# Kernel tuning notes

Hardware: AMD Instinct MI355X
Metric: run time of the kernel (lower is better)

Reference implementation:

```python
import jax, jax.numpy as jnp
import numpy as np

L, B, N, D = 8, 2, 512, 1024      # ensemble size, batch, seq, model dim
H, DH = 8, 64                      # heads, dim_head
INNER = H * DH
M = 2 * L                          # messages = [tokens, ensemble_out] concatenated on dim 0
SCALE = DH ** -0.5


def rmsnorm(x, w, eps):
    return x * jax.lax.rsqrt(jnp.mean(x * x, axis=-1, keepdims=True) + eps) * w


def setup_inputs() -> dict:
    key = jax.random.key(0)
    ks = jax.random.split(key, 8)
    bound = D ** -0.5
    tokens = jax.random.normal(ks[0], (L, B, N, D), dtype=jnp.float32)
    # per-member Linear(dim, dim): torch weight [out,in] -> stored [L, D, D]
    w_net = jax.random.uniform(ks[1], (L, D, D), jnp.float32, -bound, bound)
    b_net = jnp.zeros((L, D), jnp.float32)
    # voting attention params (stored transposed so x @ W works)
    norm_w = jnp.ones((D,), jnp.float32)
    knorm_w = jnp.ones((DH,), jnp.float32)
    wq = jax.random.uniform(ks[2], (D, INNER), jnp.float32, -bound, bound)
    wkv = jax.random.uniform(ks[3], (D, 2 * INNER), jnp.float32, -bound, bound)
    wg = jax.random.uniform(ks[4], (D, H), jnp.float32, -bound, bound)
    wout = jax.random.uniform(ks[5], (INNER, D), jnp.float32, -(INNER ** -0.5), INNER ** -0.5)
    return dict(tokens=tokens, w_net=w_net, b_net=b_net, norm_w=norm_w,
                wq=wq, wkv=wkv, knorm_w=knorm_w, wg=wg, wout=wout)


def reference(tokens, w_net, b_net, norm_w, wq, wkv, knorm_w, wg, wout):
    eps = jnp.finfo(tokens.dtype).eps
    # vmapped sub-network: per-member Linear
    out = jnp.einsum('lbnd,lod->lbno', tokens, w_net) + b_net[:, None, None, :]
    # messages = cat([tokens, out], dim=0) -> context of M=2L messages per (b,n)
    ctx = jnp.concatenate([tokens, out], axis=0)            # [M,B,N,D]
    # voting attention: queries are the tokens (len-1 per position), kv over M messages.
    # original tiles ctx over l ('m b ... d -> (lq b) ... m d'); we broadcast instead.
    tn = rmsnorm(tokens, norm_w, eps)                        # query norm only
    q = (tn @ wq).reshape(L, B, N, H, DH)
    kv = ctx @ wkv                                           # [M,B,N,2*INNER]
    k, v = jnp.split(kv, 2, axis=-1)
    k = rmsnorm(k.reshape(M, B, N, H, DH), knorm_w, eps)
    v = v.reshape(M, B, N, H, DH)
    sim = jnp.einsum('lbnhd,mbnhd->lbnhm', q, k) * SCALE
    attn = jax.nn.softmax(sim, axis=-1)
    o = jnp.einsum('lbnhm,mbnhd->lbnhd', attn, v)
    gates = jax.nn.sigmoid(tn @ wg)                          # [L,B,N,H]
    o = o * gates[..., None]
    pooled = o.reshape(L, B, N, INNER) @ wout                # [L,B,N,D]
    return pooled
```

## Files before the change

### kernel.cpp

```cpp
#include <hip/hip_runtime.h>
#include <hip/hip_bf16.h>
#include <math.h>

#define L_ 8
#define B_ 2
#define N_ 512
#define D_ 1024
#define H_ 8
#define DH_ 64
#define INNER_ 512
#define M_ 16
#define BN_TOK 1024
#define EPS 1.1920928955078125e-07f
#define SCALE_ 0.125f

typedef __attribute__((ext_vector_type(8))) __bf16 bf16x8;
typedef __attribute__((ext_vector_type(4))) __bf16 bf16x4;
typedef __attribute__((ext_vector_type(4))) float f32x4;

#define BARF() do { __builtin_amdgcn_s_barrier(); __builtin_amdgcn_sched_barrier(0); } while (0)
#define LGKM0() do { asm volatile("s_waitcnt lgkmcnt(0)" ::: "memory"); \
                     __builtin_amdgcn_sched_barrier(0); } while (0)
#define GLL(SRC, DST) __builtin_amdgcn_global_load_lds( \
    (const __attribute__((address_space(1))) void*)(SRC), \
    (__attribute__((address_space(3))) void*)(DST), 16, 0, 0)

__device__ void transpose_body(const float* __restrict__ in,
                               __bf16* __restrict__ out, int R, int C,
                               int bx, int by)
{
    __shared__ float tile[32][33];
    const int x = threadIdx.x & 31, y = threadIdx.x >> 5;
    #pragma unroll
    for (int r = 0; r < 4; ++r)
        tile[y + r * 8][x] = in[(size_t)(by * 32 + y + r * 8) * C + bx * 32 + x];
    __syncthreads();
    #pragma unroll
    for (int r = 0; r < 4; ++r)
        out[(size_t)(bx * 32 + y + r * 8) * R + by * 32 + x] = (__bf16)tile[x][y + r * 8];
}

__global__ __launch_bounds__(256) void prep_kernel(
    const float* __restrict__ tokens, const float* __restrict__ norm_w,
    const float* __restrict__ w_net, const float* __restrict__ wq,
    const float* __restrict__ wkv, const float* __restrict__ wout,
    const float* __restrict__ wg,
    __bf16* __restrict__ tok_bf, __bf16* __restrict__ tn_bf,
    __bf16* __restrict__ wnet_bf, __bf16* __restrict__ wqt,
    __bf16* __restrict__ wkvt, __bf16* __restrict__ woutt,
    __bf16* __restrict__ wgT)
{
    const int bid = blockIdx.x;
    const int t = threadIdx.x;

    if (bid < 8192) {
        const int wave = t >> 6, lane = t & 63;
        __shared__ float wsum[4];
        const float4 v = ((const float4*)(tokens + (size_t)bid * D_))[t];
        float ss = fmaf(v.x, v.x, fmaf(v.y, v.y, fmaf(v.z, v.z, v.w * v.w)));
        #pragma unroll
        for (int o = 1; o < 64; o <<= 1) ss += __shfl_xor(ss, o);
        if (lane == 0) wsum[wave] = ss;
        __syncthreads();
        const float rsv = rsqrtf((wsum[0] + wsum[1] + wsum[2] + wsum[3]) * (1.f / D_) + EPS);
        const float4 nw = ((const float4*)norm_w)[t];
        bf16x4 tb; tb.x = (__bf16)v.x; tb.y = (__bf16)v.y; tb.z = (__bf16)v.z; tb.w = (__bf16)v.w;
        ((bf16x4*)(tok_bf + (size_t)bid * D_))[t] = tb;
        bf16x4 nb;
        nb.x = (__bf16)(v.x * rsv * nw.x); nb.y = (__bf16)(v.y * rsv * nw.y);
        nb.z = (__bf16)(v.z * rsv * nw.z); nb.w = (__bf16)(v.w * rsv * nw.w);
        ((bf16x4*)(tn_bf + (size_t)bid * D_))[t] = nb;
    } else if (bid < 10240) {
        const int base = (bid - 8192) * 1024 + t;
        #pragma unroll
        for (int j = 0; j < 4; ++j) {
            const int i = base + j * 256;
            float4 v = ((const float4*)w_net)[i];
            bf16x4 o;
            o.x = (__bf16)v.x; o.y = (__bf16)v.y; o.z = (__bf16)v.z; o.w = (__bf16)v.w;
            *(bf16x4*)(wnet_bf + (size_t)i * 4) = o;
        }
    } else if (bid < 12288) {
        const int b2 = bid - 10240;
        if (b2 < 512)        transpose_body(wq, wqt, 1024, 512, b2 & 15, b2 >> 4);
        else if (b2 < 1536)  { const int b3 = b2 - 512;  transpose_body(wkv, wkvt, 1024, 1024, b3 & 31, b3 >> 5); }
        else                 { const int b3 = b2 - 1536; transpose_body(wout, woutt, 512, 1024, b3 & 31, b3 >> 5); }
    } else {
        const int g = (bid - 12288) * 256 + t;
        const int h = g >> 10, d = g & 1023;
        wgT[g] = (h < 8) ? (__bf16)wg[d * 8 + h] : (__bf16)0.f;
    }
}

__global__ __launch_bounds__(512, 2) void gemm_fused(
    const __bf16* __restrict__ tok, const __bf16* __restrict__ tn,
    const __bf16* __restrict__ wnet, const __bf16* __restrict__ wqt,
    const float* __restrict__ bias, const __bf16* __restrict__ wgT,
    __bf16* __restrict__ out_bf, __bf16* __restrict__ q_bf,
    float* __restrict__ gates_out)
{
    __shared__ __align__(16) __bf16 As[2][256 * 64];
    __shared__ __align__(16) __bf16 Bs[2][256 * 64];

    constexpr int NT = 16, K = 1024;
    const int tid = threadIdx.x;
    const int w = tid >> 6, lane = tid & 63;
    const int fr = lane & 15, fq = lane >> 4;
    const int bid = blockIdx.x;

    if (bid >= 192) {
        const int r0 = ((bid - 192) * 8 + w) * 16;
        const __bf16* arow = tn + (size_t)(r0 + fr) * D_ + fq * 8;
        const __bf16* brow = wgT + (size_t)fr * D_ + fq * 8;
        f32x4 gacc = (f32x4){0.f, 0.f, 0.f, 0.f};
        #pragma unroll 8
        for (int k0 = 0; k0 < D_; k0 += 32) {
            bf16x8 a = *(const bf16x8*)(arow + k0);
            bf16x8 b = *(const bf16x8*)(brow + k0);
            gacc = __builtin_amdgcn_mfma_f32_16x16x32_bf16(a, b, gacc, 0, 0, 0);
        }
        if (fr < 8) {
            #pragma unroll
            for (int r = 0; r < 4; ++r)
                gates_out[(size_t)(r0 + fq * 4 + r) * H_ + fr] = 1.f / (1.f + expf(-gacc[r]));
        }
        return;
    }

    const int wm = w >> 2, wn = w & 3;
    const bool isq = bid >= 128;
    const int b2 = isq ? bid - 128 : bid;
    const int ntx = isq ? 2 : 4;
    const int c = b2 & 7, s = b2 >> 3;
    const int sq = s / ntx;
    const int m0 = (c * 4 + sq) * 256;
    const int n0 = (s - sq * ntx) * 256;
    const __bf16* Ab;
    const __bf16* Btb;
    const float* biasp = nullptr;
    int Ncols;
    if (isq) {
        Ab = tn + (size_t)m0 * K; Btb = wqt + (size_t)n0 * K; Ncols = 512;
    } else {
        Ab = tok + (size_t)m0 * K;
        Btb = wnet + (size_t)(m0 >> 10) * 1024 * K + (size_t)n0 * K;
        Ncols = 1024;
        biasp = bias + (size_t)(m0 >> 10) * 1024;
    }

    const int lrow = lane >> 3;
    const int lchunk = (lane & 7) ^ lrow;
    const int fo0 = ((fq ^ (lane & 7)) << 4);
    const int fo1 = (((4 + fq) ^ (lane & 7)) << 4);

#define STAGE_A(T2, PB, HALF) do {                                            \
    _Pragma("unroll")                                                         \
    for (int ld = (HALF) * 2; ld < (HALF) * 2 + 2; ++ld)                      \
        GLL(Ab + (size_t)(w * 32 + ld * 8 + lrow) * K + (T2) * 64 + lchunk * 8, \
            &As[PB][(w * 32 + ld * 8) * 64]);                                 \
} while (0)
#define STAGE_B(T2, PB, HALF) do {                                            \
    _Pragma("unroll")                                                         \
    for (int ld = (HALF) * 2; ld < (HALF) * 2 + 2; ++ld)                      \
        GLL(Btb + (size_t)(w * 32 + ld * 8 + lrow) * K + (T2) * 64 + lchunk * 8, \
            &Bs[PB][(w * 32 + ld * 8) * 64]);                                 \
} while (0)
#define RD_A(DST, MIOFF, FO) do {                                             \
    _Pragma("unroll")                                                         \
    for (int mi = 0; mi < 4; ++mi)                                            \
        (DST)[mi] = *(const bf16x8*)(Ap + ((wm * 128 + ((MIOFF) + mi) * 16 + fr) << 7) + (FO)); \
} while (0)
#define RD_B(DST, FO) do {                                                    \
    _Pragma("unroll")                                                         \
    for (int nj = 0; nj < 4; ++nj)                                            \
        (DST)[nj] = *(const bf16x8*)(Bp + ((wn * 64 + nj * 16 + fr) << 7) + (FO)); \
} while (0)
#define MFMA16(AFR, BFR, AOFF) do {                                           \
    _Pragma("unroll")                                                         \
    for (int mi = 0; mi < 4; ++mi)                                            \
        _Pragma("unroll")                                                     \
        for (int nj = 0; nj < 4; ++nj)                                        \
            acc[(AOFF) + mi][nj] = __builtin_amdgcn_mfma_f32_16x16x32_bf16(   \
                (AFR)[mi], (BFR)[nj], acc[(AOFF) + mi][nj], 0, 0, 0);         \
} while (0)

    f32x4 acc[8][4];
    #pragma unroll
    for (int mi = 0; mi < 8; ++mi)
        #pragma unroll
        for (int nj = 0; nj < 4; ++nj)
            acc[mi][nj] = (f32x4){0.f, 0.f, 0.f, 0.f};

    STAGE_A(0, 0, 0); STAGE_A(0, 0, 1);
    STAGE_B(0, 0, 0); STAGE_B(0, 0, 1);
    STAGE_A(1, 1, 0); STAGE_A(1, 1, 1);
    asm volatile("s_waitcnt vmcnt(4)" ::: "memory");
    BARF();

    for (int t = 0; t < NT; ++t) {
        const int p = t & 1;
        const char* Ap = (const char*)&As[p][0];
        const char* Bp = (const char*)&Bs[p][0];
        bf16x8 am0k0[4], am1k0[4], bk0[4], am0k1[4], am1k1[4], bk1[4];

        RD_A(am0k0, 0, fo0); RD_B(bk0, fo0); RD_A(am1k0, 4, fo0);
        if (t + 1 < NT) STAGE_B(t + 1, p ^ 1, 0);
        BARF();
        __builtin_amdgcn_s_setprio(1);
        MFMA16(am0k0, bk0, 0);
        __builtin_amdgcn_s_setprio(0);
        BARF();

        RD_A(am0k1, 0, fo1); RD_B(bk1, fo1); RD_A(am1k1, 4, fo1);
        if (t + 1 < NT) STAGE_B(t + 1, p ^ 1, 1);
        BARF();
        __builtin_amdgcn_s_setprio(1);
        MFMA16(am1k0, bk0, 4);
        __builtin_amdgcn_s_setprio(0);
        LGKM0();
        BARF();

        if (t + 2 < NT) STAGE_A(t + 2, p, 0);
        __builtin_amdgcn_s_setprio(1);
        MFMA16(am0k1, bk1, 0);
        __builtin_amdgcn_s_setprio(0);
        BARF();

        if (t + 2 < NT) STAGE_A(t + 2, p, 1);
        __builtin_amdgcn_s_setprio(1);
        MFMA16(am1k1, bk1, 4);
        __builtin_amdgcn_s_setprio(0);
        if (t + 2 < NT) { asm volatile("s_waitcnt vmcnt(4)" ::: "memory"); }
        else            { asm volatile("s_waitcnt vmcnt(0)" ::: "memory"); }
        BARF();
    }

    #pragma unroll
    for (int mi = 0; mi < 8; ++mi) {
        const int r0 = m0 + wm * 128 + mi * 16 + fq * 4;
        #pragma unroll
        for (int nj = 0; nj < 4; ++nj) {
            const int col = n0 + wn * 64 + nj * 16 + fr;
            const float badd = (biasp != nullptr) ? biasp[col] : 0.f;
            __bf16* Co = isq ? q_bf : out_bf;
            #pragma unroll
            for (int r = 0; r < 4; ++r)
                Co[(size_t)(r0 + r) * Ncols + col] = (__bf16)(acc[mi][nj][r] + badd);
        }
    }
#undef STAGE_A
#undef STAGE_B
#undef RD_A
#undef RD_B
#undef MFMA16
}

__global__ __launch_bounds__(512, 2) void gemm_kv(
    const __bf16* __restrict__ tok, const __bf16* __restrict__ outm,
    const __bf16* __restrict__ wkvt, __bf16* __restrict__ kv_bf)
{
    __shared__ __align__(16) __bf16 As[2][256 * 64];
    __shared__ __align__(16) __bf16 Bs[2][256 * 64];
    constexpr int NT = 16, K = 1024, Ncols = 1024;
    const int tid = threadIdx.x;
    const int w = tid >> 6, lane = tid & 63;
    const int wm = w >> 2, wn = w & 3;
    const int fr = lane & 15, fq = lane >> 4;
    const int bid = blockIdx.x;
    const int c = bid & 7, s = bid >> 3;
    const int sq = s >> 2;
    const int m0 = (c * 8 + sq) * 256;
    const int n0 = (s - sq * 4) * 256;
    const __bf16* Ab = (m0 >= 8192) ? (outm + (size_t)(m0 - 8192) * K)
                                    : (tok + (size_t)m0 * K);
    const __bf16* Btb = wkvt + (size_t)n0 * K;

    const int lrow = lane >> 3;
    const int lchunk = (lane & 7) ^ lrow;
    const int fo0 = ((fq ^ (lane & 7)) << 4);
    const int fo1 = (((4 + fq) ^ (lane & 7)) << 4);

#define STAGE_A(T2, PB, HALF) do {                                            \
    _Pragma("unroll")                                                         \
    for (int ld = (HALF) * 2; ld < (HALF) * 2 + 2; ++ld)                      \
        GLL(Ab + (size_t)(w * 32 + ld * 8 + lrow) * K + (T2) * 64 + lchunk * 8, \
            &As[PB][(w * 32 + ld * 8) * 64]);                                 \
} while (0)
#define STAGE_B(T2, PB, HALF) do {                                            \
    _Pragma("unroll")                                                         \
    for (int ld = (HALF) * 2; ld < (HALF) * 2 + 2; ++ld)                      \
        GLL(Btb + (size_t)(w * 32 + ld * 8 + lrow) * K + (T2) * 64 + lchunk * 8, \
            &Bs[PB][(w * 32 + ld * 8) * 64]);                                 \
} while (0)
#define RD_A(DST, MIOFF, FO) do {                                             \
    _Pragma("unroll")                                                         \
    for (int mi = 0; mi < 4; ++mi)                                            \
        (DST)[mi] = *(const bf16x8*)(Ap + ((wm * 128 + ((MIOFF) + mi) * 16 + fr) << 7) + (FO)); \
} while (0)
#define RD_B(DST, FO) do {                                                    \
    _Pragma("unroll")                                                         \
    for (int nj = 0; nj < 4; ++nj)                                            \
        (DST)[nj] = *(const bf16x8*)(Bp + ((wn * 64 + nj * 16 + fr) << 7) + (FO)); \
} while (0)
#define MFMA16(AFR, BFR, AOFF) do {                                           \
    _Pragma("unroll")                                                         \
    for (int mi = 0; mi < 4; ++mi)                                            \
        _Pragma("unroll")                                                     \
        for (int nj = 0; nj < 4; ++nj)                                        \
            acc[(AOFF) + mi][nj] = __builtin_amdgcn_mfma_f32_16x16x32_bf16(   \
                (AFR)[mi], (BFR)[nj], acc[(AOFF) + mi][nj], 0, 0, 0);         \
} while (0)

    f32x4 acc[8][4];
    #pragma unroll
    for (int mi = 0; mi < 8; ++mi)
        #pragma unroll
        for (int nj = 0; nj < 4; ++nj)
            acc[mi][nj] = (f32x4){0.f, 0.f, 0.f, 0.f};

    STAGE_A(0, 0, 0); STAGE_A(0, 0, 1);
    STAGE_B(0, 0, 0); STAGE_B(0, 0, 1);
    STAGE_A(1, 1, 0); STAGE_A(1, 1, 1);
    asm volatile("s_waitcnt vmcnt(4)" ::: "memory");
    BARF();

    for (int t = 0; t < NT; ++t) {
        const int p = t & 1;
        const char* Ap = (const char*)&As[p][0];
        const char* Bp = (const char*)&Bs[p][0];
        bf16x8 am0k0[4], am1k0[4], bk0[4], am0k1[4], am1k1[4], bk1[4];

        RD_A(am0k0, 0, fo0); RD_B(bk0, fo0); RD_A(am1k0, 4, fo0);
        if (t + 1 < NT) STAGE_B(t + 1, p ^ 1, 0);
        BARF();
        __builtin_amdgcn_s_setprio(1);
        MFMA16(am0k0, bk0, 0);
        __builtin_amdgcn_s_setprio(0);
        BARF();

        RD_A(am0k1, 0, fo1); RD_B(bk1, fo1); RD_A(am1k1, 4, fo1);
        if (t + 1 < NT) STAGE_B(t + 1, p ^ 1, 1);
        BARF();
        __builtin_amdgcn_s_setprio(1);
        MFMA16(am1k0, bk0, 4);
        __builtin_amdgcn_s_setprio(0);
        LGKM0();
        BARF();

        if (t + 2 < NT) STAGE_A(t + 2, p, 0);
        __builtin_amdgcn_s_setprio(1);
        MFMA16(am0k1, bk1, 0);
        __builtin_amdgcn_s_setprio(0);
        BARF();

        if (t + 2 < NT) STAGE_A(t + 2, p, 1);
        __builtin_amdgcn_s_setprio(1);
        MFMA16(am1k1, bk1, 4);
        __builtin_amdgcn_s_setprio(0);
        if (t + 2 < NT) { asm volatile("s_waitcnt vmcnt(4)" ::: "memory"); }
        else            { asm volatile("s_waitcnt vmcnt(0)" ::: "memory"); }
        BARF();
    }

    #pragma unroll
    for (int mi = 0; mi < 8; ++mi) {
        const int r0 = m0 + wm * 128 + mi * 16 + fq * 4;
        #pragma unroll
        for (int nj = 0; nj < 4; ++nj) {
            const int col = n0 + wn * 64 + nj * 16 + fr;
            #pragma unroll
            for (int r = 0; r < 4; ++r)
                kv_bf[(size_t)(r0 + r) * Ncols + col] = (__bf16)acc[mi][nj][r];
        }
    }
#undef STAGE_A
#undef STAGE_B
#undef RD_A
#undef RD_B
#undef MFMA16
}

__global__ __launch_bounds__(512, 2) void gemm_final(
    const __bf16* __restrict__ A,
    const __bf16* __restrict__ Bt,
    float* __restrict__ Cf)
{
    __shared__ __align__(16) __bf16 As[2][256 * 64];
    __shared__ __align__(16) __bf16 Bs[2][128 * 64];
    constexpr int NT = 8, K = 512, Ncols = 1024;
    const int tid = threadIdx.x;
    const int w = tid >> 6, lane = tid & 63;
    const int wm = w >> 1, wn = w & 1;
    const int fr = lane & 15, fq = lane >> 4;
    const int bid = blockIdx.x;
    const int c = bid & 7, s = bid >> 3;
    const int sq = s >> 3;
    const int m0 = (c * 4 + sq) * 256;
    const int n0 = (s - sq * 8) * 128;
    const __bf16* Ab = A + (size_t)m0 * K;
    const __bf16* Btb = Bt + (size_t)n0 * K;

    const int lrow = lane >> 3;
    const int lchunk = (lane & 7) ^ lrow;
    const int fo0 = ((fq ^ (lane & 7)) << 4);
    const int fo1 = (((4 + fq) ^ (lane & 7)) << 4);

#define STAGE_A(T2, PB, HALF) do {                                            \
    _Pragma("unroll")                                                         \
    for (int ld = (HALF) * 2; ld < (HALF) * 2 + 2; ++ld)                      \
        GLL(Ab + (size_t)(w * 32 + ld * 8 + lrow) * K + (T2) * 64 + lchunk * 8, \
            &As[PB][(w * 32 + ld * 8) * 64]);                                 \
} while (0)
#define STAGE_B(T2, PB, HALF)                                                 \
    GLL(Btb + (size_t)(w * 16 + (HALF) * 8 + lrow) * K + (T2) * 64 + lchunk * 8, \
        &Bs[PB][(w * 16 + (HALF) * 8) * 64])
#define RD_A(DST, FO) do {                                                    \
    _Pragma("unroll")                                                         \
    for (int mi = 0; mi < 4; ++mi)                                            \
        (DST)[mi] = *(const bf16x8*)(Ap + ((wm * 64 + mi * 16 + fr) << 7) + (FO)); \
} while (0)
#define RD_B(DST, FO) do {                                                    \
    _Pragma("unroll")                                                         \
    for (int nj = 0; nj < 4; ++nj)                                            \
        (DST)[nj] = *(const bf16x8*)(Bp + ((wn * 64 + nj * 16 + fr) << 7) + (FO)); \
} while (0)
#define MFMA16C1(AFR, BFR) do {                                               \
    _Pragma("unroll")                                                         \
    for (int mi = 0; mi < 4; ++mi)                                            \
        _Pragma("unroll")                                                     \
        for (int nj = 0; nj < 4; ++nj)                                        \
            acc[mi][nj] = __builtin_amdgcn_mfma_f32_16x16x32_bf16(            \
                (AFR)[mi], (BFR)[nj], acc[mi][nj], 0, 0, 0);                  \
} while (0)

    f32x4 acc[4][4];
    #pragma unroll
    for (int mi = 0; mi < 4; ++mi)
        #pragma unroll
        for (int nj = 0; nj < 4; ++nj)
            acc[mi][nj] = (f32x4){0.f, 0.f, 0.f, 0.f};

    STAGE_A(0, 0, 0); STAGE_A(0, 0, 1);
    STAGE_B(0, 0, 0); STAGE_B(0, 0, 1);
    STAGE_A(1, 1, 0); STAGE_A(1, 1, 1);
    asm volatile("s_waitcnt vmcnt(4)" ::: "memory");
    BARF();

    for (int t = 0; t < NT; ++t) {
        const int p = t & 1;
        const char* Ap = (const char*)&As[p][0];
        const char* Bp = (const char*)&Bs[p][0];
        bf16x8 ak0[4], bk0[4], ak1[4], bk1[4];

        RD_A(ak0, fo0); RD_B(bk0, fo0);
        if (t + 1 < NT) STAGE_B(t + 1, p ^ 1, 0);
        BARF();
        __builtin_amdgcn_s_setprio(1);
        MFMA16C1(ak0, bk0);
        __builtin_amdgcn_s_setprio(0);
        BARF();

        RD_A(ak1, fo1); RD_B(bk1, fo1);
        if (t + 1 < NT) STAGE_B(t + 1, p ^ 1, 1);
        BARF();
        __builtin_amdgcn_s_setprio(1);
        MFMA16C1(ak1, bk1);
        __builtin_amdgcn_s_setprio(0);
        LGKM0();
        BARF();

        if (t + 2 < NT) { STAGE_A(t + 2, p, 0); STAGE_A(t + 2, p, 1); }
        if (t + 2 < NT) { asm volatile("s_waitcnt vmcnt(4)" ::: "memory"); }
        else            { asm volatile("s_waitcnt vmcnt(0)" ::: "memory"); }
        BARF();
    }

    #pragma unroll
    for (int mi = 0; mi < 4; ++mi) {
        const int r0 = m0 + wm * 64 + mi * 16 + fq * 4;
        #pragma unroll
        for (int nj = 0; nj < 4; ++nj) {
            const int col = n0 + wn * 64 + nj * 16 + fr;
            #pragma unroll
            for (int r = 0; r < 4; ++r)
                Cf[(size_t)(r0 + r) * Ncols + col] = acc[mi][nj][r];
        }
    }
#undef STAGE_A
#undef STAGE_B
#undef RD_A
#undef RD_B
#undef MFMA16C1
}

__global__ __launch_bounds__(512) void attn_kernel(
    const __bf16* __restrict__ q,
    const __bf16* __restrict__ kv,
    const float* __restrict__ gates,
    const float* __restrict__ knw,
    __bf16* __restrict__ og)
{
    const int bn = blockIdx.x;
    const int tid = threadIdx.x;
    const int h = tid >> 6, lane = tid & 63;

    __shared__ __align__(16) __bf16 qs[8][520];
    __shared__ __align__(16) __bf16 kvs[16][1032];
    __shared__ float ssm[8][8][17];
    __shared__ float kn[64];
    __shared__ float gs[64];

    {
        const int l = tid >> 6, c8 = tid & 63;
        *(bf16x8*)&qs[l][c8 * 8] =
            *(const bf16x8*)(q + ((size_t)(l * BN_TOK + bn)) * INNER_ + c8 * 8);
    }
    #pragma unroll
    for (int i = 0; i < 4; ++i) {
        const int g = tid + i * 512;
        const int m = g >> 7, c8 = g & 127;
        *(bf16x8*)&kvs[m][c8 * 8] =
            *(const bf16x8*)(kv + ((size_t)(m * BN_TOK + bn)) * 1024 + c8 * 8);
    }
    if (tid < 64) {
        kn[tid] = knw[tid];
        gs[tid] = gates[((size_t)((tid >> 3) * BN_TOK + bn)) * H_ + (tid & 7)];
    }
    __syncthreads();

    const int m = lane & 15, grp = lane >> 4;

    float s2 = 0.f;
    #pragma unroll
    for (int j = 0; j < 16; ++j) {
        float v = (float)kvs[m][h * DH_ + grp * 16 + j];
        s2 = fmaf(v, v, s2);
    }
    s2 += __shfl_xor(s2, 16);
    s2 += __shfl_xor(s2, 32);
    const float kscale = rsqrtf(s2 * (1.f / DH_) + EPS) * SCALE_;

    const int l0 = grp, l1 = grp + 4;
    float sim0 = 0.f, sim1 = 0.f;
    #pragma unroll
    for (int d = 0; d < DH_; ++d) {
        const float kf = (float)kvs[m][h * DH_ + d] * kn[d];
        sim0 = fmaf((float)qs[l0][h * DH_ + d], kf, sim0);
        sim1 = fmaf((float)qs[l1][h * DH_ + d], kf, sim1);
    }
    sim0 *= kscale; sim1 *= kscale;

    float mx0 = sim0, mx1 = sim1;
    #pragma unroll
    for (int o = 1; o < 16; o <<= 1) {
        mx0 = fmaxf(mx0, __shfl_xor(mx0, o));
        mx1 = fmaxf(mx1, __shfl_xor(mx1, o));
    }
    float e0 = expf(sim0 - mx0), e1 = expf(sim1 - mx1);
    float sm0 = e0, sm1 = e1;
    #pragma unroll
    for (int o = 1; o < 16; o <<= 1) {
        sm0 += __shfl_xor(sm0, o);
        sm1 += __shfl_xor(sm1, o);
    }
    ssm[h][l0][m] = e0 / sm0;
    ssm[h][l1][m] = e1 / sm1;

    float vf[16];
    #pragma unroll
    for (int mm = 0; mm < 16; ++mm)
        vf[mm] = (float)kvs[mm][INNER_ + h * DH_ + lane];
    #pragma unroll
    for (int l = 0; l < 8; ++l) {
        float o = 0.f;
        #pragma unroll
        for (int mm = 0; mm < 16; ++mm) o = fmaf(ssm[h][l][mm], vf[mm], o);
        og[((size_t)(l * BN_TOK + bn)) * INNER_ + h * DH_ + lane] =
            (__bf16)(o * gs[l * 8 + h]);
    }
}

extern "C" void kernel_launch(void* const* d_in, const int* in_sizes, int n_in,
                              void* d_out, int out_size, void* d_ws, size_t ws_size,
                              hipStream_t stream)
{
    const float* tokens = (const float*)d_in[0];
    const float* w_net  = (const float*)d_in[1];
    const float* b_net  = (const float*)d_in[2];
    const float* norm_w = (const float*)d_in[3];
    const float* wq     = (const float*)d_in[4];
    const float* wkv    = (const float*)d_in[5];
    const float* knw    = (const float*)d_in[6];
    const float* wg     = (const float*)d_in[7];
    const float* wout   = (const float*)d_in[8];
    float* out = (float*)d_out;

    char* ws = (char*)d_ws;
    __bf16* tok_bf  = (__bf16*)(ws);
    __bf16* tn_bf   = (__bf16*)(ws + 16777216);
    __bf16* out_bf  = (__bf16*)(ws + 33554432);
    __bf16* q_bf    = (__bf16*)(ws + 50331648);
    __bf16* kv_bf   = (__bf16*)(ws + 58720256);
    __bf16* og_bf   = (__bf16*)(ws + 92274688);
    __bf16* wnet_bf = (__bf16*)(ws + 100663296);
    __bf16* wqt_bf  = (__bf16*)(ws + 117440512);
    __bf16* wkvt_bf = (__bf16*)(ws + 118489088);
    __bf16* woutt_bf= (__bf16*)(ws + 120586240);
    float*  ws_g    = (float*)(ws + 121667584);
    __bf16* wgT_bf  = (__bf16*)(ws + 121929728);

    prep_kernel<<<12352, 256, 0, stream>>>(tokens, norm_w, w_net, wq, wkv, wout, wg,
                                           tok_bf, tn_bf, wnet_bf, wqt_bf,
                                           wkvt_bf, woutt_bf, wgT_bf);
    gemm_fused<<<256, 512, 0, stream>>>(tok_bf, tn_bf, wnet_bf, wqt_bf, b_net,
                                        wgT_bf, out_bf, q_bf, ws_g);
    gemm_kv<<<256, 512, 0, stream>>>(tok_bf, out_bf, wkvt_bf, kv_bf);
    attn_kernel<<<BN_TOK, 512, 0, stream>>>(q_bf, kv_bf, ws_g, knw, og_bf);
    gemm_final<<<256, 512, 0, stream>>>(og_bf, woutt_bf, out);
}
```

Before: 126.2 us.

## Split GEMM LDS tiles into K-halves with finer-grained staging pipeline

The shared main-loop macros for gemm_fused and gemm_kv now store each 64-wide K tile as two 32-wide halves with a new XOR swizzle. The loop is restructured into four phases, each reading one A half-fragment and issuing one staged half-tile load, instead of preloading both K halves of fragments. This cuts register pressure for fragment buffers and interleaves the global-to-LDS loads more evenly with the MFMAs. In exchange it adds more barriers and lgkm waits per iteration, and B fragments are reloaded twice per half. gemm_final is only renamed.

After: 144.3 us. 14.4% more time.

```diff
diff --git a/kernel.cpp b/kernel.cpp
--- a/kernel.cpp
+++ b/kernel.cpp
@@ -92,6 +92,94 @@
     }
 }
 
+
+#define CFG0_DECL()                                                           \
+    __shared__ __align__(16) __bf16 As[2][2][256 * 32];           \
+    __shared__ __align__(16) __bf16 Bs[2][2][256 * 32];
+
+#define CFG0_LANES()                                                          \
+    const int schunk = (lane & 3) ^ ((lane >> 3) & 3);                        \
+    const int srow = (lane >> 2);                                             \
+    const int fsw = (fq ^ ((fr >> 1) & 3)) << 4;
+
+#define STAGE_A(T2, KH, PB) do {                                              \
+    _Pragma("unroll")                                                         \
+    for (int rd = 0; rd < 2; ++rd)                                            \
+        GLL(Ab + (size_t)(rd * 128 + w * 16 + srow) * K + (T2) * 64 + (KH) * 32 + schunk * 8, \
+            &As[PB][KH][(rd * 128 + w * 16) * 32]);                           \
+} while (0)
+#define STAGE_B(T2, KH, PB) do {                                              \
+    _Pragma("unroll")                                                         \
+    for (int rd = 0; rd < 2; ++rd)                                            \
+        GLL(Btb + (size_t)(rd * 128 + w * 16 + srow) * K + (T2) * 64 + (KH) * 32 + schunk * 8, \
+            &Bs[PB][KH][(rd * 128 + w * 16) * 32]);                           \
+} while (0)
+#define RD_A4(DST, MIOFF, KHP) do {                                           \
+    _Pragma("unroll")                                                         \
+    for (int mi = 0; mi < 4; ++mi)                                            \
+        (DST)[mi] = *(const bf16x8*)((KHP) + (((wm * 128 + ((MIOFF) + mi) * 16 + fr) << 6) + fsw)); \
+} while (0)
+#define RD_B4(DST, KHP) do {                                                  \
+    _Pragma("unroll")                                                         \
+    for (int nj = 0; nj < 4; ++nj)                                            \
+        (DST)[nj] = *(const bf16x8*)((KHP) + (((wn * 64 + nj * 16 + fr) << 6) + fsw)); \
+} while (0)
+#define MFMA16(AFR, BFR, AOFF) do {                                           \
+    _Pragma("unroll")                                                         \
+    for (int mi = 0; mi < 4; ++mi)                                            \
+        _Pragma("unroll")                                                     \
+        for (int nj = 0; nj < 4; ++nj)                                        \
+            acc[(AOFF) + mi][nj] = __builtin_amdgcn_mfma_f32_16x16x32_bf16(   \
+                (AFR)[mi], (BFR)[nj], acc[(AOFF) + mi][nj], 0, 0, 0);         \
+} while (0)
+
+#define CFG0_PROLOGUE()                                                       \
+    STAGE_A(0, 0, 0); STAGE_B(0, 0, 0);                                       \
+    STAGE_A(0, 1, 0); STAGE_B(0, 1, 0);                                       \
+    STAGE_A(1, 0, 1); STAGE_B(1, 0, 1);                                       \
+    asm volatile("s_waitcnt vmcnt(4)" ::: "memory");                          \
+    BARF();
+
+#define CFG0_LOOP(NTv)                                                        \
+    for (int t = 0; t < (NTv); ++t) {                                         \
+        const int p = t & 1;                                                  \
+        const char* A0p = (const char*)&As[p][0][0];                          \
+        const char* A1p = (const char*)&As[p][1][0];                          \
+        const char* B0p = (const char*)&Bs[p][0][0];                          \
+        const char* B1p = (const char*)&Bs[p][1][0];                          \
+        bf16x8 al[4], ah[4], bb[4];                                           \
+                         \
+        RD_A4(al, 0, A0p); RD_B4(bb, B0p);                                    \
+        if (t + 1 < (NTv)) STAGE_A(t + 1, 1, p ^ 1);                          \
+        BARF(); LGKM0();                                                      \
+        __builtin_amdgcn_s_setprio(1); MFMA16(al, bb, 0);                     \
+        __builtin_amdgcn_s_setprio(0);                                        \
+        BARF();                                                               \
+                                \
+        RD_A4(ah, 4, A0p);                                                    \
+        if (t + 1 < (NTv)) STAGE_B(t + 1, 1, p ^ 1);                          \
+        BARF(); LGKM0();                                                      \
+        __builtin_amdgcn_s_setprio(1); MFMA16(ah, bb, 4);                     \
+        __builtin_amdgcn_s_setprio(0);                                        \
+        BARF();                                                               \
+          \
+        RD_A4(al, 0, A1p); RD_B4(bb, B1p);                                    \
+        if (t + 2 < (NTv)) STAGE_A(t + 2, 0, p);                              \
+        BARF(); LGKM0();                                                      \
+        __builtin_amdgcn_s_setprio(1); MFMA16(al, bb, 0);                     \
+        __builtin_amdgcn_s_setprio(0);                                        \
+        BARF();                                                               \
+                \
+        RD_A4(ah, 4, A1p);                                                    \
+        if (t + 2 < (NTv)) STAGE_B(t + 2, 0, p);                              \
+        BARF(); LGKM0();                                                      \
+        __builtin_amdgcn_s_setprio(1); MFMA16(ah, bb, 4);                     \
+        __builtin_amdgcn_s_setprio(0);                                        \
+        if (t + 2 < (NTv))      { asm volatile("s_waitcnt vmcnt(4)" ::: "memory"); } \
+        else if (t + 1 < (NTv)) { asm volatile("s_waitcnt vmcnt(0)" ::: "memory"); } \
+        BARF();                                                               \
+    }
+
 __global__ __launch_bounds__(512, 2) void gemm_fused(
     const __bf16* __restrict__ tok, const __bf16* __restrict__ tn,
     const __bf16* __restrict__ wnet, const __bf16* __restrict__ wqt,
@@ -99,9 +187,7 @@
     __bf16* __restrict__ out_bf, __bf16* __restrict__ q_bf,
     float* __restrict__ gates_out)
 {
-    __shared__ __align__(16) __bf16 As[2][256 * 64];
-    __shared__ __align__(16) __bf16 Bs[2][256 * 64];
-
+    CFG0_DECL();
     constexpr int NT = 16, K = 1024;
     const int tid = threadIdx.x;
     const int w = tid >> 6, lane = tid & 63;
@@ -148,42 +234,7 @@
         biasp = bias + (size_t)(m0 >> 10) * 1024;
     }
 
-    const int lrow = lane >> 3;
-    const int lchunk = (lane & 7) ^ lrow;
-    const int fo0 = ((fq ^ (lane & 7)) << 4);
-    const int fo1 = (((4 + fq) ^ (lane & 7)) << 4);
-
-#define STAGE_A(T2, PB, HALF) do {                                            \
-    _Pragma("unroll")                                                         \
-    for (int ld = (HALF) * 2; ld < (HALF) * 2 + 2; ++ld)                      \
-        GLL(Ab + (size_t)(w * 32 + ld * 8 + lrow) * K + (T2) * 64 + lchunk * 8, \
-            &As[PB][(w * 32 + ld * 8) * 64]);                                 \
-} while (0)
-#define STAGE_B(T2, PB, HALF) do {                                            \
-    _Pragma("unroll")                                                         \
-    for (int ld = (HALF) * 2; ld < (HALF) * 2 + 2; ++ld)                      \
-        GLL(Btb + (size_t)(w * 32 + ld * 8 + lrow) * K + (T2) * 64 + lchunk * 8, \
-            &Bs[PB][(w * 32 + ld * 8) * 64]);                                 \
-} while (0)
-#define RD_A(DST, MIOFF, FO) do {                                             \
-    _Pragma("unroll")                                                         \
-    for (int mi = 0; mi < 4; ++mi)                                            \
-        (DST)[mi] = *(const bf16x8*)(Ap + ((wm * 128 + ((MIOFF) + mi) * 16 + fr) << 7) + (FO)); \
-} while (0)
-#define RD_B(DST, FO) do {                                                    \
-    _Pragma("unroll")                                                         \
-    for (int nj = 0; nj < 4; ++nj)                                            \
-        (DST)[nj] = *(const bf16x8*)(Bp + ((wn * 64 + nj * 16 + fr) << 7) + (FO)); \
-} while (0)
-#define MFMA16(AFR, BFR, AOFF) do {                                           \
-    _Pragma("unroll")                                                         \
-    for (int mi = 0; mi < 4; ++mi)                                            \
-        _Pragma("unroll")                                                     \
-        for (int nj = 0; nj < 4; ++nj)                                        \
-            acc[(AOFF) + mi][nj] = __builtin_amdgcn_mfma_f32_16x16x32_bf16(   \
-                (AFR)[mi], (BFR)[nj], acc[(AOFF) + mi][nj], 0, 0, 0);         \
-} while (0)
-
+    CFG0_LANES();
     f32x4 acc[8][4];
     #pragma unroll
     for (int mi = 0; mi < 8; ++mi)
@@ -191,49 +242,8 @@
         for (int nj = 0; nj < 4; ++nj)
             acc[mi][nj] = (f32x4){0.f, 0.f, 0.f, 0.f};
 
-    STAGE_A(0, 0, 0); STAGE_A(0, 0, 1);
-    STAGE_B(0, 0, 0); STAGE_B(0, 0, 1);
-    STAGE_A(1, 1, 0); STAGE_A(1, 1, 1);
-    asm volatile("s_waitcnt vmcnt(4)" ::: "memory");
-    BARF();
-
-    for (int t = 0; t < NT; ++t) {
-        const int p = t & 1;
-        const char* Ap = (const char*)&As[p][0];
-        const char* Bp = (const char*)&Bs[p][0];
-        bf16x8 am0k0[4], am1k0[4], bk0[4], am0k1[4], am1k1[4], bk1[4];
-
-        RD_A(am0k0, 0, fo0); RD_B(bk0, fo0); RD_A(am1k0, 4, fo0);
-        if (t + 1 < NT) STAGE_B(t + 1, p ^ 1, 0);
-        BARF();
-        __builtin_amdgcn_s_setprio(1);
-        MFMA16(am0k0, bk0, 0);
-        __builtin_amdgcn_s_setprio(0);
-        BARF();
-
-        RD_A(am0k1, 0, fo1); RD_B(bk1, fo1); RD_A(am1k1, 4, fo1);
-        if (t + 1 < NT) STAGE_B(t + 1, p ^ 1, 1);
-        BARF();
-        __builtin_amdgcn_s_setprio(1);
-        MFMA16(am1k0, bk0, 4);
-        __builtin_amdgcn_s_setprio(0);
-        LGKM0();
-        BARF();
-
-        if (t + 2 < NT) STAGE_A(t + 2, p, 0);
-        __builtin_amdgcn_s_setprio(1);
-        MFMA16(am0k1, bk1, 0);
-        __builtin_amdgcn_s_setprio(0);
-        BARF();
-
-        if (t + 2 < NT) STAGE_A(t + 2, p, 1);
-        __builtin_amdgcn_s_setprio(1);
-        MFMA16(am1k1, bk1, 4);
-        __builtin_amdgcn_s_setprio(0);
-        if (t + 2 < NT) { asm volatile("s_waitcnt vmcnt(4)" ::: "memory"); }
-        else            { asm volatile("s_waitcnt vmcnt(0)" ::: "memory"); }
-        BARF();
-    }
+    CFG0_PROLOGUE();
+    CFG0_LOOP(NT);
 
     #pragma unroll
     for (int mi = 0; mi < 8; ++mi) {
@@ -248,19 +258,13 @@
                 Co[(size_t)(r0 + r) * Ncols + col] = (__bf16)(acc[mi][nj][r] + badd);
         }
     }
-#undef STAGE_A
-#undef STAGE_B
-#undef RD_A
-#undef RD_B
-#undef MFMA16
 }
 
 __global__ __launch_bounds__(512, 2) void gemm_kv(
     const __bf16* __restrict__ tok, const __bf16* __restrict__ outm,
     const __bf16* __restrict__ wkvt, __bf16* __restrict__ kv_bf)
 {
-    __shared__ __align__(16) __bf16 As[2][256 * 64];
-    __shared__ __align__(16) __bf16 Bs[2][256 * 64];
+    CFG0_DECL();
     constexpr int NT = 16, K = 1024, Ncols = 1024;
     const int tid = threadIdx.x;
     const int w = tid >> 6, lane = tid & 63;
@@ -275,42 +279,7 @@
                                     : (tok + (size_t)m0 * K);
     const __bf16* Btb = wkvt + (size_t)n0 * K;
 
-    const int lrow = lane >> 3;
-    const int lchunk = (lane & 7) ^ lrow;
-    const int fo0 = ((fq ^ (lane & 7)) << 4);
-    const int fo1 = (((4 + fq) ^ (lane & 7)) << 4);
-
-#define STAGE_A(T2, PB, HALF) do {                                            \
-    _Pragma("unroll")                                                         \
-    for (int ld = (HALF) * 2; ld < (HALF) * 2 + 2; ++ld)                      \
-        GLL(Ab + (size_t)(w * 32 + ld * 8 + lrow) * K + (T2) * 64 + lchunk * 8, \
-            &As[PB][(w * 32 + ld * 8) * 64]);                                 \
-} while (0)
-#define STAGE_B(T2, PB, HALF) do {                                            \
-    _Pragma("unroll")                                                         \
-    for (int ld = (HALF) * 2; ld < (HALF) * 2 + 2; ++ld)                      \
-        GLL(Btb + (size_t)(w * 32 + ld * 8 + lrow) * K + (T2) * 64 + lchunk * 8, \
-            &Bs[PB][(w * 32 + ld * 8) * 64]);                                 \
-} while (0)
-#define RD_A(DST, MIOFF, FO) do {                                             \
-    _Pragma("unroll")                                                         \
-    for (int mi = 0; mi < 4; ++mi)                                            \
-        (DST)[mi] = *(const bf16x8*)(Ap + ((wm * 128 + ((MIOFF) + mi) * 16 + fr) << 7) + (FO)); \
-} while (0)
-#define RD_B(DST, FO) do {                                                    \
-    _Pragma("unroll")                                                         \
-    for (int nj = 0; nj < 4; ++nj)                                            \
-        (DST)[nj] = *(const bf16x8*)(Bp + ((wn * 64 + nj * 16 + fr) << 7) + (FO)); \
-} while (0)
-#define MFMA16(AFR, BFR, AOFF) do {                                           \
-    _Pragma("unroll")                                                         \
-    for (int mi = 0; mi < 4; ++mi)                                            \
-        _Pragma("unroll")                                                     \
-        for (int nj = 0; nj < 4; ++nj)                                        \
-            acc[(AOFF) + mi][nj] = __builtin_amdgcn_mfma_f32_16x16x32_bf16(   \
-                (AFR)[mi], (BFR)[nj], acc[(AOFF) + mi][nj], 0, 0, 0);         \
-} while (0)
-
+    CFG0_LANES();
     f32x4 acc[8][4];
     #pragma unroll
     for (int mi = 0; mi < 8; ++mi)
@@ -318,49 +287,8 @@
         for (int nj = 0; nj < 4; ++nj)
             acc[mi][nj] = (f32x4){0.f, 0.f, 0.f, 0.f};
 
-    STAGE_A(0, 0, 0); STAGE_A(0, 0, 1);
-    STAGE_B(0, 0, 0); STAGE_B(0, 0, 1);
-    STAGE_A(1, 1, 0); STAGE_A(1, 1, 1);
-    asm volatile("s_waitcnt vmcnt(4)" ::: "memory");
-    BARF();
-
-    for (int t = 0; t < NT; ++t) {
-        const int p = t & 1;
-        const char* Ap = (const char*)&As[p][0];
-        const char* Bp = (const char*)&Bs[p][0];
-        bf16x8 am0k0[4], am1k0[4], bk0[4], am0k1[4], am1k1[4], bk1[4];
-
-        RD_A(am0k0, 0, fo0); RD_B(bk0, fo0); RD_A(am1k0, 4, fo0);
-        if (t + 1 < NT) STAGE_B(t + 1, p ^ 1, 0);
-        BARF();
-        __builtin_amdgcn_s_setprio(1);
-        MFMA16(am0k0, bk0, 0);
-        __builtin_amdgcn_s_setprio(0);
-        BARF();
-
-        RD_A(am0k1, 0, fo1); RD_B(bk1, fo1); RD_A(am1k1, 4, fo1);
-        if (t + 1 < NT) STAGE_B(t + 1, p ^ 1, 1);
-        BARF();
-        __builtin_amdgcn_s_setprio(1);
-        MFMA16(am1k0, bk0, 4);
-        __builtin_amdgcn_s_setprio(0);
-        LGKM0();
-        BARF();
-
-        if (t + 2 < NT) STAGE_A(t + 2, p, 0);
-        __builtin_amdgcn_s_setprio(1);
-        MFMA16(am0k1, bk1, 0);
-        __builtin_amdgcn_s_setprio(0);
-        BARF();
-
-        if (t + 2 < NT) STAGE_A(t + 2, p, 1);
-        __builtin_amdgcn_s_setprio(1);
-        MFMA16(am1k1, bk1, 4);
-        __builtin_amdgcn_s_setprio(0);
-        if (t + 2 < NT) { asm volatile("s_waitcnt vmcnt(4)" ::: "memory"); }
-        else            { asm volatile("s_waitcnt vmcnt(0)" ::: "memory"); }
-        BARF();
-    }
+    CFG0_PROLOGUE();
+    CFG0_LOOP(NT);
 
     #pragma unroll
     for (int mi = 0; mi < 8; ++mi) {
@@ -373,20 +301,18 @@
                 kv_bf[(size_t)(r0 + r) * Ncols + col] = (__bf16)acc[mi][nj][r];
         }
     }
+}
+
 #undef STAGE_A
 #undef STAGE_B
-#undef RD_A
-#undef RD_B
-#undef MFMA16
-}
 
 __global__ __launch_bounds__(512, 2) void gemm_final(
     const __bf16* __restrict__ A,
     const __bf16* __restrict__ Bt,
     float* __restrict__ Cf)
 {
-    __shared__ __align__(16) __bf16 As[2][256 * 64];
-    __shared__ __align__(16) __bf16 Bs[2][128 * 64];
+    __shared__ __align__(16) __bf16 Asf[2][256 * 64];
+    __shared__ __align__(16) __bf16 Bsf[2][128 * 64];
     constexpr int NT = 8, K = 512, Ncols = 1024;
     const int tid = threadIdx.x;
     const int w = tid >> 6, lane = tid & 63;
@@ -405,26 +331,26 @@
     const int fo0 = ((fq ^ (lane & 7)) << 4);
     const int fo1 = (((4 + fq) ^ (lane & 7)) << 4);
 
-#define STAGE_A(T2, PB, HALF) do {                                            \
+#define F_STAGE_A(T2, PB, HALF) do {                                          \
     _Pragma("unroll")                                                         \
     for (int ld = (HALF) * 2; ld < (HALF) * 2 + 2; ++ld)                      \
         GLL(Ab + (size_t)(w * 32 + ld * 8 + lrow) * K + (T2) * 64 + lchunk * 8, \
-            &As[PB][(w * 32 + ld * 8) * 64]);                                 \
-} while (0)
-#define STAGE_B(T2, PB, HALF)                                                 \
+            &Asf[PB][(w * 32 + ld * 8) * 64]);                                \
+} while (0)
+#define F_STAGE_B(T2, PB, HALF)                                               \
     GLL(Btb + (size_t)(w * 16 + (HALF) * 8 + lrow) * K + (T2) * 64 + lchunk * 8, \
-        &Bs[PB][(w * 16 + (HALF) * 8) * 64])
-#define RD_A(DST, FO) do {                                                    \
+        &Bsf[PB][(w * 16 + (HALF) * 8) * 64])
+#define F_RD_A(DST, FO) do {                                                  \
     _Pragma("unroll")                                                         \
     for (int mi = 0; mi < 4; ++mi)                                            \
         (DST)[mi] = *(const bf16x8*)(Ap + ((wm * 64 + mi * 16 + fr) << 7) + (FO)); \
 } while (0)
-#define RD_B(DST, FO) do {                                                    \
+#define F_RD_B(DST, FO) do {                                                  \
     _Pragma("unroll")                                                         \
     for (int nj = 0; nj < 4; ++nj)                                            \
         (DST)[nj] = *(const bf16x8*)(Bp + ((wn * 64 + nj * 16 + fr) << 7) + (FO)); \
 } while (0)
-#define MFMA16C1(AFR, BFR) do {                                               \
+#define F_MFMA16(AFR, BFR) do {                                               \
     _Pragma("unroll")                                                         \
     for (int mi = 0; mi < 4; ++mi)                                            \
         _Pragma("unroll")                                                     \
@@ -440,36 +366,36 @@
         for (int nj = 0; nj < 4; ++nj)
             acc[mi][nj] = (f32x4){0.f, 0.f, 0.f, 0.f};
 
-    STAGE_A(0, 0, 0); STAGE_A(0, 0, 1);
-    STAGE_B(0, 0, 0); STAGE_B(0, 0, 1);
-    STAGE_A(1, 1, 0); STAGE_A(1, 1, 1);
+    F_STAGE_A(0, 0, 0); F_STAGE_A(0, 0, 1);
+    F_STAGE_B(0, 0, 0); F_STAGE_B(0, 0, 1);
+    F_STAGE_A(1, 1, 0); F_STAGE_A(1, 1, 1);
     asm volatile("s_waitcnt vmcnt(4)" ::: "memory");
     BARF();
 
     for (int t = 0; t < NT; ++t) {
         const int p = t & 1;
-        const char* Ap = (const char*)&As[p][0];
-        const char* Bp = (const char*)&Bs[p][0];
+        const char* Ap = (const char*)&Asf[p][0];
+        const char* Bp = (const char*)&Bsf[p][0];
         bf16x8 ak0[4], bk0[4], ak1[4], bk1[4];
 
-        RD_A(ak0, fo0); RD_B(bk0, fo0);
-        if (t + 1 < NT) STAGE_B(t + 1, p ^ 1, 0);
+        F_RD_A(ak0, fo0); F_RD_B(bk0, fo0);
+        if (t + 1 < NT) F_STAGE_B(t + 1, p ^ 1, 0);
         BARF();
         __builtin_amdgcn_s_setprio(1);
-        MFMA16C1(ak0, bk0);
+        F_MFMA16(ak0, bk0);
         __builtin_amdgcn_s_setprio(0);
         BARF();
 
-        RD_A(ak1, fo1); RD_B(bk1, fo1);
-        if (t + 1 < NT) STAGE_B(t + 1, p ^ 1, 1);
+        F_RD_A(ak1, fo1); F_RD_B(bk1, fo1);
+        if (t + 1 < NT) F_STAGE_B(t + 1, p ^ 1, 1);
         BARF();
         __builtin_amdgcn_s_setprio(1);
-        MFMA16C1(ak1, bk1);
+        F_MFMA16(ak1, bk1);
         __builtin_amdgcn_s_setprio(0);
         LGKM0();
         BARF();
 
-        if (t + 2 < NT) { STAGE_A(t + 2, p, 0); STAGE_A(t + 2, p, 1); }
+        if (t + 2 < NT) { F_STAGE_A(t + 2, p, 0); F_STAGE_A(t + 2, p, 1); }
         if (t + 2 < NT) { asm volatile("s_waitcnt vmcnt(4)" ::: "memory"); }
         else            { asm volatile("s_waitcnt vmcnt(0)" ::: "memory"); }
         BARF();
@@ -486,11 +412,11 @@
                 Cf[(size_t)(r0 + r) * Ncols + col] = acc[mi][nj][r];
         }
     }
-#undef STAGE_A
-#undef STAGE_B
-#undef RD_A
-#undef RD_B
-#undef MFMA16C1
+#undef F_STAGE_A
+#undef F_STAGE_B
+#undef F_RD_A
+#undef F_RD_B
+#undef F_MFMA16
 }
 
 __global__ __launch_bounds__(512) void attn_kernel(
```
